# Optimization experiments

Measured on AMD Instinct MI355X. Metric: run time of the kernel, lower is better.

## Reference

```python
import jax, jax.numpy as jnp
import numpy as np

# Config values (from c.mean_shift / c.cuda in the original module)
EMBED_DIM = 32      # embedding_dim
BW = 2.0            # kernel_bandwidth
ETA = 0.5           # step_size
N_ITERS = 3         # nb_iterations
RES = 96            # pic_res (image is RES x RES, N = RES*RES pixels)


def setup_inputs() -> dict:
    key = jax.random.key(0)
    # Scale 0.1 keeps exp(BW * x^T x) well inside fp32 range, mimicking the
    # bounded embeddings produced by the upstream margin-loss-trained net.
    x_in = 0.1 * jax.random.normal(key, (1, EMBED_DIM, RES, RES), dtype=jnp.float32)
    return {"x_in": x_in}


def reference(x_in):
    # x_in: (1, D, RES, RES). One mean-shift step per iteration:
    #   K = exp(bw * X^T X)                      (N x N affinity)
    #   deg_j = sum_i K[i, j]                    (column degree; K is symmetric)
    #   X_new = eta * X @ (K / deg) + (1-eta) * X
    # (The original's torch.inverse(diag(deg)) is exactly 1/deg column scaling.)
    # All iterates are concatenated along dim 0, as in the torch code.
    res = x_in.shape[3]
    n = res * res
    xs = [x_in.reshape(EMBED_DIM, n)]
    for _ in range(N_ITERS):
        X = xs[-1]                                    # (D, N)
        K = jnp.exp(BW * jnp.einsum('di,dj->ij', X, X))  # (N, N)
        deg = K.sum(axis=0)                           # (N,) column sums
        xs.append(ETA * (X @ (K / deg)) + (1.0 - ETA) * X)
    # (N_ITERS+1, D, RES, RES)
    return jnp.stack(xs, axis=0).reshape(-1, EMBED_DIM, res, res)
```

## Files before the change

kernel.cpp:

```cpp
#include <hip/hip_runtime.h>
#include <hip/hip_bf16.h>


#define DIM 32
#define RESO 96
#define NPT (RESO * RESO)
#define NITER 3
#define ETA 0.5f
#define SCALE 2.88539008f

#define QB 128
#define NWAVE 4
#define NQB (NPT / QB)
#define KSEG 14
#define NCHUNK_TOT (NPT / 64)
#define PSTRIDE 72

typedef __bf16 bf16_t;
typedef __bf16 v8bf __attribute__((ext_vector_type(8)));
typedef float  v4f  __attribute__((ext_vector_type(4)));

__global__ void pack_kernel(const float* __restrict__ X,
                            bf16_t* __restrict__ rows,
                            bf16_t* __restrict__ cols,
                            float* __restrict__ out_copy) {
    int idx = blockIdx.x * 256 + threadIdx.x;
    if (idx >= DIM * NPT) return;
    int d = idx / NPT;
    int n = idx - d * NPT;
    float v = X[idx];
    cols[idx] = (bf16_t)v;
    rows[n * DIM + d] = (bf16_t)v;
    out_copy[idx] = v;
}

__global__ __launch_bounds__(256, 4)
void msattn_kernel(const float* __restrict__ Xcur,
                   const bf16_t* __restrict__ rows,
                   const bf16_t* __restrict__ cols,
                   float* __restrict__ part_num,
                   float* __restrict__ part_den) {
    __shared__ __align__(16) bf16_t tiles[2][4096];
    __shared__ __align__(16) bf16_t pslab[NWAVE][32 * PSTRIDE];

    const int tid  = threadIdx.x;
    const int w    = tid >> 6;
    const int lane = tid & 63;
    const int quad = lane >> 4;
    const int l16  = lane & 15;
    const int qb   = blockIdx.x;
    const int ks   = blockIdx.y;
    const int c0   = (NCHUNK_TOT * ks) / KSEG;
    const int c1   = (NCHUNK_TOT * (ks + 1)) / KSEG;
    const int q0w  = qb * QB + w * 32;

    bf16_t* p_lds = pslab[w];

    v8bf afrag0, afrag1;
#pragma unroll
    for (int j = 0; j < 8; ++j) {
        const float* src = Xcur + (quad * 8 + j) * NPT + q0w + l16;
        afrag0[j] = (bf16_t)(src[0] * SCALE);
        afrag1[j] = (bf16_t)(src[16] * SCALE);
    }

    const bf16_t* gsrc[2];
    int gdelta[2], ldst[2];
#pragma unroll
    for (int i = 0; i < 2; ++i) {
        int p = 2 * w + i;
        if (p < 4) {
            gsrc[i] = rows + ((size_t)c0 * 64 + 4 * l16 + p) * DIM + quad * 8;
            gdelta[i] = 64 * DIM;
            ldst[i] = p * 512 + lane * 8;
        } else {
            int r = p - 4, h = r >> 1, g = r & 1;
            gsrc[i] = cols + (size_t)(h * 16 + l16) * NPT + c0 * 64 + g * 32 + quad * 8;
            gdelta[i] = 64;
            ldst[i] = 2048 + r * 512 + lane * 8;
        }
    }

    v4f acc00 = {0.f, 0.f, 0.f, 0.f};
    v4f acc01 = {0.f, 0.f, 0.f, 0.f};
    v4f acc10 = {0.f, 0.f, 0.f, 0.f};
    v4f acc11 = {0.f, 0.f, 0.f, 0.f};
    float den0[4] = {0.f, 0.f, 0.f, 0.f};
    float den1[4] = {0.f, 0.f, 0.f, 0.f};

#pragma unroll
    for (int i = 0; i < 2; ++i) {
        v8bf st = *(const v8bf*)gsrc[i];
        gsrc[i] += gdelta[i];
        *(v8bf*)&tiles[0][ldst[i]] = st;
    }
    __syncthreads();

    for (int c = c0; c < c1; ++c) {
        const int cc = c - c0;
        const bf16_t* tb = tiles[cc & 1];
        const bool more = (c + 1 < c1);

        v8bf stn0, stn1;
        if (more) {
            stn0 = *(const v8bf*)gsrc[0]; gsrc[0] += gdelta[0];
            stn1 = *(const v8bf*)gsrc[1]; gsrc[1] += gdelta[1];
        }

        v4f s0[4], s1[4];
#pragma unroll
        for (int t = 0; t < 4; ++t) {
            v8bf b = *(const v8bf*)&tb[t * 512 + lane * 8];
            s0[t] = __builtin_amdgcn_mfma_f32_16x16x32_bf16(afrag0, b,
                                                            (v4f){0.f, 0.f, 0.f, 0.f}, 0, 0, 0);
            s1[t] = __builtin_amdgcn_mfma_f32_16x16x32_bf16(afrag1, b,
                                                            (v4f){0.f, 0.f, 0.f, 0.f}, 0, 0, 0);
        }

#pragma unroll
        for (int r = 0; r < 4; ++r) {
            union { bf16_t h[4]; unsigned long long u; } pk0, pk1;
#pragma unroll
            for (int t = 0; t < 4; ++t) {
                float w0 = __builtin_amdgcn_exp2f(s0[t][r]);
                float w1 = __builtin_amdgcn_exp2f(s1[t][r]);
                den0[r] += w0; den1[r] += w1;
                pk0.h[t] = (bf16_t)w0; pk1.h[t] = (bf16_t)w1;
            }
            *(unsigned long long*)&p_lds[(quad * 4 + r) * PSTRIDE + 4 * l16] = pk0.u;
            *(unsigned long long*)&p_lds[(16 + quad * 4 + r) * PSTRIDE + 4 * l16] = pk1.u;
        }

        v8bf b00 = *(const v8bf*)&tb[2048 + 0 * 512 + lane * 8];
        v8bf b01 = *(const v8bf*)&tb[2048 + 1 * 512 + lane * 8];
        v8bf b10 = *(const v8bf*)&tb[2048 + 2 * 512 + lane * 8];
        v8bf b11 = *(const v8bf*)&tb[2048 + 3 * 512 + lane * 8];
        {
            v8bf a20 = *(const v8bf*)&p_lds[l16 * PSTRIDE + quad * 8];
            v8bf a21 = *(const v8bf*)&p_lds[l16 * PSTRIDE + 32 + quad * 8];
            acc00 = __builtin_amdgcn_mfma_f32_16x16x32_bf16(a20, b00, acc00, 0, 0, 0);
            acc01 = __builtin_amdgcn_mfma_f32_16x16x32_bf16(a20, b10, acc01, 0, 0, 0);
            acc00 = __builtin_amdgcn_mfma_f32_16x16x32_bf16(a21, b01, acc00, 0, 0, 0);
            acc01 = __builtin_amdgcn_mfma_f32_16x16x32_bf16(a21, b11, acc01, 0, 0, 0);
        }
        {
            v8bf a20 = *(const v8bf*)&p_lds[(16 + l16) * PSTRIDE + quad * 8];
            v8bf a21 = *(const v8bf*)&p_lds[(16 + l16) * PSTRIDE + 32 + quad * 8];
            acc10 = __builtin_amdgcn_mfma_f32_16x16x32_bf16(a20, b00, acc10, 0, 0, 0);
            acc11 = __builtin_amdgcn_mfma_f32_16x16x32_bf16(a20, b10, acc11, 0, 0, 0);
            acc10 = __builtin_amdgcn_mfma_f32_16x16x32_bf16(a21, b01, acc10, 0, 0, 0);
            acc11 = __builtin_amdgcn_mfma_f32_16x16x32_bf16(a21, b11, acc11, 0, 0, 0);
        }

        if (more) {
            *(v8bf*)&tiles[(cc + 1) & 1][ldst[0]] = stn0;
            *(v8bf*)&tiles[(cc + 1) & 1][ldst[1]] = stn1;
        }
        __syncthreads();
    }

#pragma unroll
    for (int m = 1; m < 16; m <<= 1) {
#pragma unroll
        for (int r = 0; r < 4; ++r) {
            den0[r] += __shfl_xor(den0[r], m);
            den1[r] += __shfl_xor(den1[r], m);
        }
    }
    float* pn = part_num + (size_t)ks * NPT * DIM;
#pragma unroll
    for (int r = 0; r < 4; ++r) {
        int gq0 = q0w + quad * 4 + r;
        int gq1 = gq0 + 16;
        pn[(size_t)gq0 * DIM + l16]      = acc00[r];
        pn[(size_t)gq0 * DIM + 16 + l16] = acc01[r];
        pn[(size_t)gq1 * DIM + l16]      = acc10[r];
        pn[(size_t)gq1 * DIM + 16 + l16] = acc11[r];
    }
    if (l16 == 0) {
#pragma unroll
        for (int r = 0; r < 4; ++r) {
            part_den[ks * NPT + q0w + quad * 4 + r]      = den0[r];
            part_den[ks * NPT + q0w + 16 + quad * 4 + r] = den1[r];
        }
    }
}

__global__ __launch_bounds__(256, 4)
void reduce_kernel(const float* __restrict__ part_num,
                   const float* __restrict__ part_den,
                   const float* __restrict__ Xcur,
                   float* __restrict__ Xnext,
                   bf16_t* __restrict__ rows_out,
                   bf16_t* __restrict__ cols_out) {
    __shared__ float tnum[32][33];
    __shared__ float txn[32][33];
    __shared__ float tden[32];

    const int tid = threadIdx.x;
    const int q0  = blockIdx.x * 32;

#pragma unroll
    for (int j = 0; j < 4; ++j) {
        int idx = tid + j * 256;
        int qq = idx >> 5, d = idx & 31;
        float s = 0.f;
#pragma unroll
        for (int ss = 0; ss < KSEG; ++ss)
            s += part_num[((size_t)ss * NPT + q0 + qq) * DIM + d];
        tnum[qq][d] = s;
    }
    if (tid < 32) {
        float s = 0.f;
#pragma unroll
        for (int ss = 0; ss < KSEG; ++ss)
            s += part_den[ss * NPT + q0 + tid];
        tden[tid] = s;
    }
    __syncthreads();

#pragma unroll
    for (int j = 0; j < 4; ++j) {
        int idx = tid + j * 256;
        int d = idx >> 5, qq = idx & 31;
        float num = tnum[qq][d];
        float dn  = tden[qq];
        float xo  = Xcur[d * NPT + q0 + qq];
        float xn  = ETA * num / dn + (1.0f - ETA) * xo;
        Xnext[d * NPT + q0 + qq] = xn;
        cols_out[(size_t)d * NPT + q0 + qq] = (bf16_t)xn;
        txn[qq][d] = xn;
    }
    __syncthreads();

#pragma unroll
    for (int j = 0; j < 4; ++j) {
        int idx = tid + j * 256;
        int qq = idx >> 5, d = idx & 31;
        rows_out[(size_t)(q0 + qq) * DIM + d] = (bf16_t)txn[qq][d];
    }
}

extern "C" void kernel_launch(void* const* d_in, const int* in_sizes, int n_in,
                              void* d_out, int out_size, void* d_ws, size_t ws_size,
                              hipStream_t stream) {
    const float* x_in = (const float*)d_in[0];
    float* out = (float*)d_out;

    const size_t DN = (size_t)DIM * NPT;
    bf16_t* rows0 = (bf16_t*)d_ws;
    bf16_t* cols0 = rows0 + DN;
    bf16_t* rows1 = cols0 + DN;
    bf16_t* cols1 = rows1 + DN;
    float* part_num = (float*)(cols1 + DN);
    float* part_den = part_num + (size_t)KSEG * NPT * DIM;

    const int pack_blocks = (DIM * NPT + 255) / 256;
    pack_kernel<<<pack_blocks, 256, 0, stream>>>(x_in, rows0, cols0, out);

    for (int it = 0; it < NITER; ++it) {
        const float* Xcur = (it == 0) ? x_in : out + (size_t)it * DN;
        bf16_t* rin  = (it & 1) ? rows1 : rows0;
        bf16_t* cin  = (it & 1) ? cols1 : cols0;
        bf16_t* rout = (it & 1) ? rows0 : rows1;
        bf16_t* cout = (it & 1) ? cols0 : cols1;
        msattn_kernel<<<dim3(NQB, KSEG), 256, 0, stream>>>(Xcur, rin, cin,
                                                           part_num, part_den);
        reduce_kernel<<<NPT / 32, 256, 0, stream>>>(part_num, part_den, Xcur,
                                                    out + (size_t)(it + 1) * DN,
                                                    rout, cout);
    }
}
```

Baseline: 147.7 us.

## Double query block to 8 waves and compute degree sums via MFMA with ones

Grows each block to 256 queries and 8 waves and halves the key-segment split, so every wave loads one staged vector per chunk instead of two and each shared K/V tile is reused by twice as many queries. Column-degree sums move off VALU adds and the final cross-lane shuffle reduction onto extra MFMAs against a ones vector. The cost is summing from bf16-rounded weights, which is slightly less precise, plus fewer blocks in the grid and larger blocks that can lower occupancy.

```diff
diff --git a/kernel.cpp b/kernel.cpp
--- a/kernel.cpp
+++ b/kernel.cpp
@@ -9,10 +9,10 @@
 #define ETA 0.5f
 #define SCALE 2.88539008f
 
-#define QB 128
-#define NWAVE 4
+#define QB 256
+#define NWAVE 8
 #define NQB (NPT / QB)
-#define KSEG 14
+#define KSEG 7
 #define NCHUNK_TOT (NPT / 64)
 #define PSTRIDE 72
 
@@ -34,7 +34,7 @@
     out_copy[idx] = v;
 }
 
-__global__ __launch_bounds__(256, 4)
+__global__ __launch_bounds__(512, 2)
 void msattn_kernel(const float* __restrict__ Xcur,
                    const bf16_t* __restrict__ rows,
                    const bf16_t* __restrict__ cols,
@@ -64,35 +64,34 @@
         afrag1[j] = (bf16_t)(src[16] * SCALE);
     }
 
-    const bf16_t* gsrc[2];
-    int gdelta[2], ldst[2];
-#pragma unroll
-    for (int i = 0; i < 2; ++i) {
-        int p = 2 * w + i;
-        if (p < 4) {
-            gsrc[i] = rows + ((size_t)c0 * 64 + 4 * l16 + p) * DIM + quad * 8;
-            gdelta[i] = 64 * DIM;
-            ldst[i] = p * 512 + lane * 8;
-        } else {
-            int r = p - 4, h = r >> 1, g = r & 1;
-            gsrc[i] = cols + (size_t)(h * 16 + l16) * NPT + c0 * 64 + g * 32 + quad * 8;
-            gdelta[i] = 64;
-            ldst[i] = 2048 + r * 512 + lane * 8;
-        }
+    v8bf ones;
+#pragma unroll
+    for (int j = 0; j < 8; ++j) ones[j] = (bf16_t)1.0f;
+
+    const bf16_t* gsrc;
+    int gdelta, ldst;
+    if (w < 4) {
+        gsrc = rows + ((size_t)c0 * 64 + 4 * l16 + w) * DIM + quad * 8;
+        gdelta = 64 * DIM;
+        ldst = w * 512 + lane * 8;
+    } else {
+        int r = w - 4, h = r >> 1, g = r & 1;
+        gsrc = cols + (size_t)(h * 16 + l16) * NPT + c0 * 64 + g * 32 + quad * 8;
+        gdelta = 64;
+        ldst = 2048 + r * 512 + lane * 8;
     }
 
     v4f acc00 = {0.f, 0.f, 0.f, 0.f};
     v4f acc01 = {0.f, 0.f, 0.f, 0.f};
     v4f acc10 = {0.f, 0.f, 0.f, 0.f};
     v4f acc11 = {0.f, 0.f, 0.f, 0.f};
-    float den0[4] = {0.f, 0.f, 0.f, 0.f};
-    float den1[4] = {0.f, 0.f, 0.f, 0.f};
-
-#pragma unroll
-    for (int i = 0; i < 2; ++i) {
-        v8bf st = *(const v8bf*)gsrc[i];
-        gsrc[i] += gdelta[i];
-        *(v8bf*)&tiles[0][ldst[i]] = st;
+    v4f dden0 = {0.f, 0.f, 0.f, 0.f};
+    v4f dden1 = {0.f, 0.f, 0.f, 0.f};
+
+    {
+        v8bf st = *(const v8bf*)gsrc;
+        gsrc += gdelta;
+        *(v8bf*)&tiles[0][ldst] = st;
     }
     __syncthreads();
 
@@ -101,11 +100,8 @@
         const bf16_t* tb = tiles[cc & 1];
         const bool more = (c + 1 < c1);
 
-        v8bf stn0, stn1;
-        if (more) {
-            stn0 = *(const v8bf*)gsrc[0]; gsrc[0] += gdelta[0];
-            stn1 = *(const v8bf*)gsrc[1]; gsrc[1] += gdelta[1];
-        }
+        v8bf stn;
+        if (more) { stn = *(const v8bf*)gsrc; gsrc += gdelta; }
 
         v4f s0[4], s1[4];
 #pragma unroll
@@ -122,10 +118,8 @@
             union { bf16_t h[4]; unsigned long long u; } pk0, pk1;
 #pragma unroll
             for (int t = 0; t < 4; ++t) {
-                float w0 = __builtin_amdgcn_exp2f(s0[t][r]);
-                float w1 = __builtin_amdgcn_exp2f(s1[t][r]);
-                den0[r] += w0; den1[r] += w1;
-                pk0.h[t] = (bf16_t)w0; pk1.h[t] = (bf16_t)w1;
+                pk0.h[t] = (bf16_t)__builtin_amdgcn_exp2f(s0[t][r]);
+                pk1.h[t] = (bf16_t)__builtin_amdgcn_exp2f(s1[t][r]);
             }
             *(unsigned long long*)&p_lds[(quad * 4 + r) * PSTRIDE + 4 * l16] = pk0.u;
             *(unsigned long long*)&p_lds[(16 + quad * 4 + r) * PSTRIDE + 4 * l16] = pk1.u;
@@ -142,6 +136,8 @@
             acc01 = __builtin_amdgcn_mfma_f32_16x16x32_bf16(a20, b10, acc01, 0, 0, 0);
             acc00 = __builtin_amdgcn_mfma_f32_16x16x32_bf16(a21, b01, acc00, 0, 0, 0);
             acc01 = __builtin_amdgcn_mfma_f32_16x16x32_bf16(a21, b11, acc01, 0, 0, 0);
+            dden0 = __builtin_amdgcn_mfma_f32_16x16x32_bf16(a20, ones, dden0, 0, 0, 0);
+            dden0 = __builtin_amdgcn_mfma_f32_16x16x32_bf16(a21, ones, dden0, 0, 0, 0);
         }
         {
             v8bf a20 = *(const v8bf*)&p_lds[(16 + l16) * PSTRIDE + quad * 8];
@@ -150,23 +146,14 @@
             acc11 = __builtin_amdgcn_mfma_f32_16x16x32_bf16(a20, b10, acc11, 0, 0, 0);
             acc10 = __builtin_amdgcn_mfma_f32_16x16x32_bf16(a21, b01, acc10, 0, 0, 0);
             acc11 = __builtin_amdgcn_mfma_f32_16x16x32_bf16(a21, b11, acc11, 0, 0, 0);
-        }
-
-        if (more) {
-            *(v8bf*)&tiles[(cc + 1) & 1][ldst[0]] = stn0;
-            *(v8bf*)&tiles[(cc + 1) & 1][ldst[1]] = stn1;
-        }
+            dden1 = __builtin_amdgcn_mfma_f32_16x16x32_bf16(a20, ones, dden1, 0, 0, 0);
+            dden1 = __builtin_amdgcn_mfma_f32_16x16x32_bf16(a21, ones, dden1, 0, 0, 0);
+        }
+
+        if (more) *(v8bf*)&tiles[(cc + 1) & 1][ldst] = stn;
         __syncthreads();
     }
 
-#pragma unroll
-    for (int m = 1; m < 16; m <<= 1) {
-#pragma unroll
-        for (int r = 0; r < 4; ++r) {
-            den0[r] += __shfl_xor(den0[r], m);
-            den1[r] += __shfl_xor(den1[r], m);
-        }
-    }
     float* pn = part_num + (size_t)ks * NPT * DIM;
 #pragma unroll
     for (int r = 0; r < 4; ++r) {
@@ -180,8 +167,8 @@
     if (l16 == 0) {
 #pragma unroll
         for (int r = 0; r < 4; ++r) {
-            part_den[ks * NPT + q0w + quad * 4 + r]      = den0[r];
-            part_den[ks * NPT + q0w + 16 + quad * 4 + r] = den1[r];
+            part_den[ks * NPT + q0w + quad * 4 + r]      = dden0[r];
+            part_den[ks * NPT + q0w + 16 + quad * 4 + r] = dden1[r];
         }
     }
 }
@@ -264,7 +251,7 @@
         bf16_t* cin  = (it & 1) ? cols1 : cols0;
         bf16_t* rout = (it & 1) ? rows0 : rows1;
         bf16_t* cout = (it & 1) ? cols0 : cols1;
-        msattn_kernel<<<dim3(NQB, KSEG), 256, 0, stream>>>(Xcur, rin, cin,
+        msattn_kernel<<<dim3(NQB, KSEG), 512, 0, stream>>>(Xcur, rin, cin,
                                                            part_num, part_den);
         reduce_kernel<<<NPT / 32, 256, 0, stream>>>(part_num, part_den, Xcur,
                                                     out + (size_t)(it + 1) * DN,
```

Result: faster. 138.5 us (-6.2%).
